# Kernel tuning notes

Measured on AMD Instinct MI355X. Metric: run time of the kernel, lower is better.

The kernel has to match this reference:

```python
import jax, jax.numpy as jnp
import numpy as np

V, D, T_BLK, H, L = 32000, 1024, 1024, 8 * 2, 8
HD = D // H
B, T = 4, 1024
EPS = 1e-5


def _ln(x, g, b):
    mu = jnp.mean(x, axis=-1, keepdims=True)
    var = jnp.mean(jnp.square(x - mu), axis=-1, keepdims=True)
    return (x - mu) * jax.lax.rsqrt(var + EPS) * g + b


def _forward(idx, tok_emb, pos_emb, Wq, Wk, Wv, Wo, bo, ln1_g, ln1_b, ln2_g, ln2_b,
             W1, b1, W2, b2, lnf_g, lnf_b, Whead, bhead):
    Bc, Tc = idx.shape
    x = tok_emb[idx] + pos_emb[:Tc]          # [B,T,D]
    mask = jnp.tril(jnp.ones((Tc, Tc), dtype=bool))
    scale = HD ** -0.5

    def block(x, p):
        wq, wk, wv, wo, bo_, g1, be1, g2, be2, w1, bf1, w2, bf2 = p
        xn = _ln(x, g1, be1)
        # per-head no-bias projections: wq/wk/wv are [H, D, HD]
        q = jnp.einsum('btd,hde->bhte', xn, wq)
        k = jnp.einsum('btd,hde->bhte', xn, wk)
        v = jnp.einsum('btd,hde->bhte', xn, wv)
        scores = jnp.einsum('bhte,bhse->bhts', q, k) * scale
        scores = jnp.where(mask, scores, -jnp.inf)
        w = jax.nn.softmax(scores, axis=-1)
        o = jnp.einsum('bhts,bhse->bhte', w, v)             # [B,H,T,HD]
        o = o.transpose(0, 2, 1, 3).reshape(Bc, Tc, D)       # concat heads
        x = x + jnp.einsum('btd,de->bte', o, wo) + bo_
        xn2 = _ln(x, g2, be2)
        h = jax.nn.gelu(jnp.einsum('btd,df->btf', xn2, w1) + bf1, approximate=False)
        x = x + jnp.einsum('btf,fd->btd', h, w2) + bf2
        return x, None

    x, _ = jax.lax.scan(block, x, (Wq, Wk, Wv, Wo, bo, ln1_g, ln1_b, ln2_g, ln2_b,
                                   W1, b1, W2, b2))
    x = _ln(x, lnf_g, lnf_b)
    logits = jnp.einsum('btd,dv->btv', x, Whead) + bhead
    return logits


def setup_inputs() -> dict:
    key = jax.random.key(0)
    ks = jax.random.split(key, 16)
    s = 0.02
    inp = {
        'idx': jax.random.randint(ks[0], (B, T), 0, V),
        'tok_emb': jax.random.normal(ks[1], (V, D), jnp.float32) * s,
        'pos_emb': jax.random.normal(ks[2], (T_BLK, D), jnp.float32) * s,
        'Wq': jax.random.normal(ks[3], (L, H, D, HD), jnp.float32) * s,
        'Wk': jax.random.normal(ks[4], (L, H, D, HD), jnp.float32) * s,
        'Wv': jax.random.normal(ks[5], (L, H, D, HD), jnp.float32) * s,
        'Wo': jax.random.normal(ks[6], (L, D, D), jnp.float32) * s,
        'bo': jnp.zeros((L, D), jnp.float32),
        'ln1_g': jnp.ones((L, D), jnp.float32),
        'ln1_b': jnp.zeros((L, D), jnp.float32),
        'ln2_g': jnp.ones((L, D), jnp.float32),
        'ln2_b': jnp.zeros((L, D), jnp.float32),
        'W1': jax.random.normal(ks[7], (L, D, 4 * D), jnp.float32) * s,
        'b1': jnp.zeros((L, 4 * D), jnp.float32),
        'W2': jax.random.normal(ks[8], (L, 4 * D, D), jnp.float32) * s,
        'b2': jnp.zeros((L, D), jnp.float32),
        'lnf_g': jnp.ones((D,), jnp.float32),
        'lnf_b': jnp.zeros((D,), jnp.float32),
        'Whead': jax.random.normal(ks[9], (D, V), jnp.float32) * s,
        'bhead': jnp.zeros((V,), jnp.float32),
    }
    return inp


def reference(idx, tok_emb, pos_emb, Wq, Wk, Wv, Wo, bo, ln1_g, ln1_b, ln2_g, ln2_b,
              W1, b1, W2, b2, lnf_g, lnf_b, Whead, bhead):
    return _forward(idx, tok_emb, pos_emb, Wq, Wk, Wv, Wo, bo, ln1_g, ln1_b,
                    ln2_g, ln2_b, W1, b1, W2, b2, lnf_g, lnf_b, Whead, bhead)
```

## Files before the change

### kernel.cpp

```cpp
#include <hip/hip_runtime.h>
#include <hip/hip_bf16.h>

typedef short bf16x8 __attribute__((ext_vector_type(8)));
typedef float f32x4 __attribute__((ext_vector_type(4)));

__device__ __forceinline__ unsigned short f2bf(float f) {
  union { float f; unsigned u; } un; un.f = f;
  unsigned r = un.u + 0x7fffu + ((un.u >> 16) & 1u);
  return (unsigned short)(r >> 16);
}

__device__ __forceinline__ void gl_lds16(const void* g, void* l) {
  __builtin_amdgcn_global_load_lds(
      (const __attribute__((address_space(1))) void*)g,
      (__attribute__((address_space(3))) void*)l, 16, 0, 0);
}

__global__ __launch_bounds__(256) void embed_k(const int* __restrict__ idx,
                                               const float* __restrict__ tok,
                                               const float* __restrict__ pos,
                                               float* __restrict__ x) {
  int m = blockIdx.x, t = threadIdx.x;
  int tk = idx[m];
  int tp = m & 1023;
  float4 a = ((const float4*)(tok + (long)tk * 1024))[t];
  float4 p = ((const float4*)(pos + (long)tp * 1024))[t];
  a.x += p.x; a.y += p.y; a.z += p.z; a.w += p.w;
  ((float4*)(x + (long)m * 1024))[t] = a;
}

__global__ __launch_bounds__(256) void ln_k(const float* __restrict__ x,
                                            const float* __restrict__ g,
                                            const float* __restrict__ b,
                                            unsigned short* __restrict__ out) {
  int row = blockIdx.x, t = threadIdx.x;
  float4 v = ((const float4*)(x + (long)row * 1024))[t];
  float s = v.x + v.y + v.z + v.w;
  float ss = v.x * v.x + v.y * v.y + v.z * v.z + v.w * v.w;
#pragma unroll
  for (int d = 32; d; d >>= 1) { s += __shfl_xor(s, d, 64); ss += __shfl_xor(ss, d, 64); }
  __shared__ float red[8];
  int wave = t >> 6, lane = t & 63;
  if (lane == 0) { red[wave] = s; red[wave + 4] = ss; }
  __syncthreads();
  s = red[0] + red[1] + red[2] + red[3];
  ss = red[4] + red[5] + red[6] + red[7];
  float mu = s * (1.f / 1024.f);
  float var = ss * (1.f / 1024.f) - mu * mu;
  float rstd = rsqrtf(var + 1e-5f);
  float4 gv = ((const float4*)g)[t];
  float4 bv = ((const float4*)b)[t];
  ushort4 o;
  o.x = f2bf((v.x - mu) * rstd * gv.x + bv.x);
  o.y = f2bf((v.y - mu) * rstd * gv.y + bv.y);
  o.z = f2bf((v.z - mu) * rstd * gv.z + bv.z);
  o.w = f2bf((v.w - mu) * rstd * gv.w + bv.w);
  ((ushort4*)(out + (long)row * 1024))[t] = o;
}

__global__ __launch_bounds__(256) void tr_k(const float* __restrict__ in,
                                            unsigned short* __restrict__ out,
                                            int R, int C, long inStride, long outStride) {
  __shared__ float tile[32][33];
  int batch = blockIdx.z;
  int c0 = blockIdx.x * 32, r0 = blockIdx.y * 32;
  const float* ip = in + (long)batch * inStride;
  unsigned short* op = out + (long)batch * outStride;
  int tx = threadIdx.x, ty = threadIdx.y;
#pragma unroll
  for (int i = 0; i < 4; ++i)
    tile[ty + i * 8][tx] = ip[(long)(r0 + ty + i * 8) * C + c0 + tx];
  __syncthreads();
#pragma unroll
  for (int i = 0; i < 4; ++i)
    op[(long)(c0 + ty + i * 8) * R + r0 + tx] = f2bf(tile[tx][ty + i * 8]);
}

__global__ __launch_bounds__(256) void tr_qkv_k(const float* __restrict__ wq,
                                                const float* __restrict__ wk,
                                                const float* __restrict__ wv,
                                                unsigned short* __restrict__ out) {
  __shared__ float tile[32][33];
  int z = blockIdx.z;
  int tsel = z >> 7, rem = z & 127;
  int l = rem >> 4, h = rem & 15;
  const float* ip = (tsel == 0 ? wq : tsel == 1 ? wk : wv) + (long)rem * 65536;
  unsigned short* op = out + (long)l * (3072 * 1024) + (long)tsel * (1024 * 1024) +
                       (long)h * 65536;
  int c0 = blockIdx.x * 32, r0 = blockIdx.y * 32;
  int tx = threadIdx.x, ty = threadIdx.y;
#pragma unroll
  for (int i = 0; i < 4; ++i)
    tile[ty + i * 8][tx] = ip[(long)(r0 + ty + i * 8) * 64 + c0 + tx];
  __syncthreads();
#pragma unroll
  for (int i = 0; i < 4; ++i)
    op[(long)(c0 + ty + i * 8) * 1024 + r0 + tx] = f2bf(tile[tx][ty + i * 8]);
}

template <int EPI>
__global__ __launch_bounds__(256) void gemm_bt(const unsigned short* __restrict__ A,
                                               const unsigned short* __restrict__ Bt,
                                               float* __restrict__ outf,
                                               unsigned short* __restrict__ outb,
                                               const float* __restrict__ bias,
                                               const float* __restrict__ res,
                                               int M, int N, int K) {
  __shared__ __align__(16) unsigned short sA[128 * 64];
  __shared__ __align__(16) unsigned short sB[128 * 64];
  const int t = threadIdx.x;
  const int wave = t >> 6, lane = t & 63;

  const int gx = gridDim.x;
  const int nwg = gx * gridDim.y;
  const int bid = blockIdx.y * gx + blockIdx.x;
  const int qd = nwg >> 3, rd = nwg & 7;
  const int xcd = bid & 7, off = bid >> 3;
  const int swz = (xcd < rd ? xcd * (qd + 1) : rd * (qd + 1) + (xcd - rd) * qd) + off;
  const int m0 = (swz / gx) << 7, n0 = (swz % gx) << 7;

  const int wm = (wave >> 1) * 64, wn = (wave & 1) * 64;
  const f32x4 z4 = {0.f, 0.f, 0.f, 0.f};
  f32x4 acc[4][4];
#pragma unroll
  for (int i = 0; i < 4; ++i)
#pragma unroll
    for (int j = 0; j < 4; ++j) acc[i][j] = z4;

  const int srow = t >> 3;
  const int scb = (((t & 7) ^ ((t >> 3) & 7)) << 4);
  const char* Ab = (const char*)A;
  const char* Bb = (const char*)Bt;
  char* sAb = (char*)sA;
  char* sBb = (char*)sB;
  const long ldb2 = (long)K * 2;
  const int pc0 = (((lane >> 4) ^ (lane & 7)) << 4);

  for (int k0 = 0; k0 < K; k0 += 64) {
    __syncthreads();
#pragma unroll
    for (int i = 0; i < 4; ++i) {
      int row = i * 32 + srow;
      gl_lds16(Ab + (long)(m0 + row) * ldb2 + (long)k0 * 2 + scb,
               sAb + i * 4096 + wave * 1024);
      gl_lds16(Bb + (long)(n0 + row) * ldb2 + (long)k0 * 2 + scb,
               sBb + i * 4096 + wave * 1024);
    }
    __syncthreads();
#pragma unroll
    for (int kk = 0; kk < 2; ++kk) {
      const int kb = pc0 ^ (kk << 6);
      bf16x8 af[4], bfr[4];
#pragma unroll
      for (int f = 0; f < 4; ++f) {
        int ra = wm + f * 16 + (lane & 15);
        af[f] = *(const bf16x8*)(sAb + ra * 128 + kb);
        int rb = wn + f * 16 + (lane & 15);
        bfr[f] = *(const bf16x8*)(sBb + rb * 128 + kb);
      }
#pragma unroll
      for (int fm = 0; fm < 4; ++fm)
#pragma unroll
        for (int fn = 0; fn < 4; ++fn)
          acc[fm][fn] = __builtin_amdgcn_mfma_f32_16x16x32_bf16(af[fm], bfr[fn], acc[fm][fn], 0, 0, 0);
    }
  }
  const int rl = (lane >> 4) << 2;
  const int cl = lane & 15;
#pragma unroll
  for (int fm = 0; fm < 4; ++fm) {
#pragma unroll
    for (int fn = 0; fn < 4; ++fn) {
#pragma unroll
      for (int r = 0; r < 4; ++r) {
        int m = m0 + wm + fm * 16 + rl + r;
        int n = n0 + wn + fn * 16 + cl;
        float v = acc[fm][fn][r];
        if (EPI == 1 || EPI == 2 || EPI == 3) v += bias[n];
        if (EPI == 1) v += res[(long)m * N + n];
        if (EPI == 2) v = 0.5f * v * (1.f + erff(v * 0.70710678118f));
        if (EPI == 0 || EPI == 2) outb[(long)m * N + n] = f2bf(v);
        else outf[(long)m * N + n] = v;
      }
    }
  }
}

__global__ __launch_bounds__(256) void attn_k(const unsigned short* __restrict__ qkv,
                                              unsigned short* __restrict__ o) {
  const int qt = blockIdx.x;
  const int pair = blockIdx.y;
  const int b = pair >> 4, h = pair & 15;
  const int t = threadIdx.x, wave = t >> 6, lane = t & 63;
  __shared__ __align__(16) unsigned short sQ[64 * 64];
  __shared__ __align__(16) unsigned short sK[64 * 64];
  __shared__ __align__(16) unsigned short sV[64 * 64];
  __shared__ __align__(16) unsigned short sP[4][16 * 64];

  const long baseq = (long)b * (1024 * 3072) + (long)h * 64;
  const unsigned short* qp = qkv + baseq;
  const unsigned short* kp = qkv + baseq + 1024;
  const unsigned short* vp = qkv + baseq + 2048;
  const long baseo = (long)b * (1024 * 1024) + (long)h * 64;

  {
    int c = t;
#pragma unroll
    for (int it = 0; it < 2; ++it, c += 256) {
      int row = c >> 3, e0 = (c & 7) << 3;
      bf16x8 val = *(const bf16x8*)(qp + (long)(qt * 64 + row) * 3072 + e0);
      *(bf16x8*)((char*)sQ + row * 128 + ((e0 * 2) ^ ((row & 7) << 4))) = val;
    }
  }

  float mst[4], lst[4];
  const f32x4 z4 = {0.f, 0.f, 0.f, 0.f};
  f32x4 oacc[4];
#pragma unroll
  for (int r = 0; r < 4; ++r) { mst[r] = -1e30f; lst[r] = 0.f; }
#pragma unroll
  for (int eb = 0; eb < 4; ++eb) oacc[eb] = z4;

  for (int kt = 0; kt <= qt; ++kt) {
    __syncthreads();
    {
      int c = t;
#pragma unroll
      for (int it = 0; it < 2; ++it, c += 256) {
        int row = c >> 3, e0 = (c & 7) << 3;
        bf16x8 kv = *(const bf16x8*)(kp + (long)(kt * 64 + row) * 3072 + e0);
        *(bf16x8*)((char*)sK + row * 128 + ((e0 * 2) ^ ((row & 7) << 4))) = kv;
        bf16x8 vv = *(const bf16x8*)(vp + (long)(kt * 64 + row) * 3072 + e0);
#pragma unroll
        for (int j = 0; j < 8; ++j) {
          int e = e0 + j;
          *(unsigned short*)((char*)sV + e * 128 + ((row * 2) ^ ((e & 7) << 4))) =
              (unsigned short)vv[j];
        }
      }
    }
    __syncthreads();

    f32x4 sf[4];
#pragma unroll
    for (int cb = 0; cb < 4; ++cb) {
      f32x4 s = z4;
#pragma unroll
      for (int kk = 0; kk < 2; ++kk) {
        int e0 = (kk * 32 + ((lane >> 4) << 3)) * 2;
        int qr = wave * 16 + (lane & 15);
        bf16x8 aq = *(const bf16x8*)((char*)sQ + qr * 128 + (e0 ^ ((qr & 7) << 4)));
        int kr = cb * 16 + (lane & 15);
        bf16x8 bk = *(const bf16x8*)((char*)sK + kr * 128 + (e0 ^ ((kr & 7) << 4)));
        s = __builtin_amdgcn_mfma_f32_16x16x32_bf16(aq, bk, s, 0, 0, 0);
      }
      sf[cb] = s;
    }

    const bool diag = (kt == qt);
#pragma unroll
    for (int r = 0; r < 4; ++r) {
      int qg = wave * 16 + ((lane >> 4) << 2) + r;
      float mx = -1e30f;
#pragma unroll
      for (int cb = 0; cb < 4; ++cb) {
        float sv = sf[cb][r] * 0.125f;
        if (diag) {
          int kg = cb * 16 + (lane & 15);
          if (kg > qg) sv = -1e30f;
        }
        sf[cb][r] = sv;
        mx = fmaxf(mx, sv);
      }
#pragma unroll
      for (int d = 1; d < 16; d <<= 1) mx = fmaxf(mx, __shfl_xor(mx, d, 64));
      float mnew = fmaxf(mst[r], mx);
      float corr = __expf(mst[r] - mnew);
      mst[r] = mnew;
      float rs = 0.f;
#pragma unroll
      for (int cb = 0; cb < 4; ++cb) {
        float p = __expf(sf[cb][r] - mnew);
        sf[cb][r] = p;
        rs += p;
      }
#pragma unroll
      for (int d = 1; d < 16; d <<= 1) rs += __shfl_xor(rs, d, 64);
      lst[r] = lst[r] * corr + rs;
#pragma unroll
      for (int eb = 0; eb < 4; ++eb) oacc[eb][r] *= corr;
    }

    unsigned short* pb = sP[wave];
#pragma unroll
    for (int r = 0; r < 4; ++r) {
      int lr = ((lane >> 4) << 2) + r;
#pragma unroll
      for (int cb = 0; cb < 4; ++cb) {
        int col = cb * 16 + (lane & 15);
        *(unsigned short*)((char*)pb + lr * 128 + ((col * 2) ^ ((lr & 7) << 4))) =
            f2bf(sf[cb][r]);
      }
    }

#pragma unroll
    for (int eb = 0; eb < 4; ++eb) {
#pragma unroll
      for (int kk = 0; kk < 2; ++kk) {
        int j0 = (kk * 32 + ((lane >> 4) << 3)) * 2;
        int pr = lane & 15;
        bf16x8 ap = *(const bf16x8*)((char*)pb + pr * 128 + (j0 ^ ((pr & 7) << 4)));
        int er = eb * 16 + (lane & 15);
        bf16x8 bv = *(const bf16x8*)((char*)sV + er * 128 + (j0 ^ ((er & 7) << 4)));
        oacc[eb] = __builtin_amdgcn_mfma_f32_16x16x32_bf16(ap, bv, oacc[eb], 0, 0, 0);
      }
    }
  }

#pragma unroll
  for (int r = 0; r < 4; ++r) {
    float inv = 1.f / lst[r];
    int qg = qt * 64 + wave * 16 + ((lane >> 4) << 2) + r;
#pragma unroll
    for (int eb = 0; eb < 4; ++eb) {
      int e = eb * 16 + (lane & 15);
      o[baseo + (long)qg * 1024 + e] = f2bf(oacc[eb][r] * inv);
    }
  }
}

extern "C" void kernel_launch(void* const* d_in, const int* in_sizes, int n_in,
                              void* d_out, int out_size, void* d_ws, size_t ws_size,
                              hipStream_t stream) {
  const int* idx = (const int*)d_in[0];
  const float* tok = (const float*)d_in[1];
  const float* pos = (const float*)d_in[2];
  const float* Wq = (const float*)d_in[3];
  const float* Wk = (const float*)d_in[4];
  const float* Wv = (const float*)d_in[5];
  const float* Wo = (const float*)d_in[6];
  const float* bo = (const float*)d_in[7];
  const float* ln1g = (const float*)d_in[8];
  const float* ln1b = (const float*)d_in[9];
  const float* ln2g = (const float*)d_in[10];
  const float* ln2b = (const float*)d_in[11];
  const float* W1 = (const float*)d_in[12];
  const float* b1 = (const float*)d_in[13];
  const float* W2 = (const float*)d_in[14];
  const float* b2 = (const float*)d_in[15];
  const float* lnfg = (const float*)d_in[16];
  const float* lnfb = (const float*)d_in[17];
  const float* Wh = (const float*)d_in[18];
  const float* bh = (const float*)d_in[19];

  char* ws = (char*)d_ws;
  const long Mi = 1024 * 1024;
  float* x = (float*)ws;
  unsigned short* xn = (unsigned short*)(ws + 16 * Mi);
  unsigned short* qkv = (unsigned short*)(ws + 24 * Mi);
  unsigned short* ob = (unsigned short*)(ws + 48 * Mi);
  unsigned short* hmid = (unsigned short*)(ws + 24 * Mi);
  unsigned short* wqkvT = (unsigned short*)(ws + 56 * Mi);
  unsigned short* wot = (unsigned short*)(ws + 104 * Mi);
  unsigned short* w1t = (unsigned short*)(ws + 106 * Mi);
  unsigned short* w2t = (unsigned short*)(ws + 114 * Mi);
  unsigned short* whT = (unsigned short*)(ws + 56 * Mi);

  dim3 blk256(256), blkT(32, 8);

  embed_k<<<4096, blk256, 0, stream>>>(idx, tok, pos, x);
  tr_qkv_k<<<dim3(2, 32, 384), blkT, 0, stream>>>(Wq, Wk, Wv, wqkvT);

  for (int l = 0; l < 8; ++l) {
    const float* wo_l = Wo + (long)l * 1048576;
    const float* w1_l = W1 + (long)l * 4194304;
    const float* w2_l = W2 + (long)l * 4194304;
    const float* bo_l = bo + (long)l * 1024;
    const float* b1_l = b1 + (long)l * 4096;
    const float* b2_l = b2 + (long)l * 1024;
    const unsigned short* wqkv_l = wqkvT + (long)l * (3072 * 1024);

    tr_k<<<dim3(32, 32, 1), blkT, 0, stream>>>(wo_l, wot, 1024, 1024, 0, 0);
    tr_k<<<dim3(128, 32, 1), blkT, 0, stream>>>(w1_l, w1t, 1024, 4096, 0, 0);
    tr_k<<<dim3(32, 128, 1), blkT, 0, stream>>>(w2_l, w2t, 4096, 1024, 0, 0);

    ln_k<<<4096, blk256, 0, stream>>>(x, ln1g + l * 1024, ln1b + l * 1024, xn);

    gemm_bt<0><<<dim3(24, 32), blk256, 0, stream>>>(xn, wqkv_l, nullptr, qkv, nullptr, nullptr, 4096, 3072, 1024);

    attn_k<<<dim3(16, 64), blk256, 0, stream>>>(qkv, ob);

    gemm_bt<1><<<dim3(8, 32), blk256, 0, stream>>>(ob, wot, x, nullptr, bo_l, x, 4096, 1024, 1024);

    ln_k<<<4096, blk256, 0, stream>>>(x, ln2g + l * 1024, ln2b + l * 1024, xn);

    gemm_bt<2><<<dim3(32, 32), blk256, 0, stream>>>(xn, w1t, nullptr, hmid, b1_l, nullptr, 4096, 4096, 1024);
    gemm_bt<1><<<dim3(8, 32), blk256, 0, stream>>>(hmid, w2t, x, nullptr, b2_l, x, 4096, 1024, 4096);
  }

  ln_k<<<4096, blk256, 0, stream>>>(x, lnfg, lnfb, xn);
  tr_k<<<dim3(1000, 32, 1), blkT, 0, stream>>>(Wh, whT, 1024, 32000, 0, 0);
  gemm_bt<3><<<dim3(250, 32), blk256, 0, stream>>>(xn, whT, (float*)d_out, nullptr, bh, nullptr, 4096, 32000, 1024);
}
```

Measured before the change: 2.904 ms.

## Add 256x256 tile, 8-wave GEMM with 4-stage LDS pipeline for QKV/FFN1/head

Adds a 512-thread GEMM kernel that computes 256x256 output tiles. It uses a four-deep global-to-LDS prefetch ring with split A/B staging, XCD-aware block swizzling and MFMA priority hints. The QKV, FFN up-projection and LM-head GEMMs move to it, and gemm_bt's epilogue is trimmed to the residual and bf16 cases it still serves. The aim is more data reuse per tile and better latency hiding, at the cost of high register and LDS use (one block per CU) and fewer blocks for small grids.

```diff
diff --git a/kernel.cpp b/kernel.cpp
--- a/kernel.cpp
+++ b/kernel.cpp
@@ -176,11 +176,131 @@
         int m = m0 + wm + fm * 16 + rl + r;
         int n = n0 + wn + fn * 16 + cl;
         float v = acc[fm][fn][r];
-        if (EPI == 1 || EPI == 2 || EPI == 3) v += bias[n];
-        if (EPI == 1) v += res[(long)m * N + n];
+        if (EPI == 1) v += bias[n] + res[(long)m * N + n];
+        if (EPI == 1) outf[(long)m * N + n] = v;
+        else outb[(long)m * N + n] = f2bf(v);
+      }
+    }
+  }
+}
+
+template <int EPI>
+__global__ __launch_bounds__(512, 1) void gemm256(const unsigned short* __restrict__ A,
+                                                  const unsigned short* __restrict__ Bt,
+                                                  float* __restrict__ outf,
+                                                  unsigned short* __restrict__ outb,
+                                                  const float* __restrict__ bias,
+                                                  int M, int N, int K) {
+  __shared__ __align__(16) char smem[131072];
+  const int t = threadIdx.x;
+  const int wave = t >> 6, lane = t & 63;
+
+  const int gx = gridDim.x;
+  const int nwg = gx * gridDim.y;
+  const int bid = blockIdx.y * gx + blockIdx.x;
+  const int qd = nwg >> 3, rd = nwg & 7;
+  const int xcd = bid & 7, off = bid >> 3;
+  const int swz = (xcd < rd ? xcd * (qd + 1) : rd * (qd + 1) + (xcd - rd) * qd) + off;
+  const int m0 = (swz / gx) << 8, n0 = (swz % gx) << 8;
+
+  const int wm = (wave >> 2) << 7;
+  const int wn = (wave & 3) << 6;
+  const int KT = K >> 5;
+
+  const f32x4 z4 = {0.f, 0.f, 0.f, 0.f};
+  f32x4 acc[8][4];
+#pragma unroll
+  for (int i = 0; i < 8; ++i)
+#pragma unroll
+    for (int j = 0; j < 4; ++j) acc[i][j] = z4;
+
+  const int srow = t >> 2;
+  const int sck = (((t & 3) ^ ((t >> 3) & 3)) << 4);
+  const long ldb = (long)K * 2;
+  const char* Asrc = (const char*)A + (long)(m0 + srow) * ldb + sck;
+  const char* Asrc2 = Asrc + 128 * ldb;
+  const char* Bsrc = (const char*)Bt + (long)(n0 + srow) * ldb + sck;
+  const char* Bsrc2 = Bsrc + 128 * ldb;
+
+#define STAGE_A(tt)                                                     \
+  { char* d = smem + ((tt) & 3) * 32768 + wave * 1024;                  \
+    long ko = (long)(tt) * 64;                                          \
+    gl_lds16(Asrc + ko, d); gl_lds16(Asrc2 + ko, d + 8192); }
+#define STAGE_B(tt)                                                     \
+  { char* d = smem + ((tt) & 3) * 32768 + 16384 + wave * 1024;          \
+    long ko = (long)(tt) * 64;                                          \
+    gl_lds16(Bsrc + ko, d); gl_lds16(Bsrc2 + ko, d + 8192); }
+
+  STAGE_A(0); STAGE_B(0);
+  STAGE_A(1); STAGE_B(1);
+  STAGE_A(2); STAGE_B(2);
+  asm volatile("s_waitcnt vmcnt(8)" ::: "memory");
+  __builtin_amdgcn_sched_barrier(0);
+  __builtin_amdgcn_s_barrier();
+
+  const int pck16 = (((lane >> 4) ^ ((lane >> 1) & 3)) << 4);
+  const int la15 = lane & 15;
+
+  for (int tt = 0; tt < KT; ++tt) {
+    const char* bA = smem + (tt & 3) * 32768;
+    const char* bB = bA + 16384;
+    bf16x8 af[4], bfr[4];
+
+#pragma unroll
+    for (int f = 0; f < 4; ++f)
+      af[f] = *(const bf16x8*)(bA + (wm + f * 16 + la15) * 64 + pck16);
+#pragma unroll
+    for (int g = 0; g < 4; ++g)
+      bfr[g] = *(const bf16x8*)(bB + (wn + g * 16 + la15) * 64 + pck16);
+    if (tt + 3 < KT) STAGE_A(tt + 3);
+    __builtin_amdgcn_s_barrier();
+    __builtin_amdgcn_s_setprio(1);
+#pragma unroll
+    for (int fm = 0; fm < 4; ++fm)
+#pragma unroll
+      for (int fn = 0; fn < 4; ++fn)
+        acc[fm][fn] = __builtin_amdgcn_mfma_f32_16x16x32_bf16(af[fm], bfr[fn], acc[fm][fn], 0, 0, 0);
+    __builtin_amdgcn_s_setprio(0);
+    __builtin_amdgcn_s_barrier();
+
+#pragma unroll
+    for (int f = 0; f < 4; ++f)
+      af[f] = *(const bf16x8*)(bA + (wm + (f + 4) * 16 + la15) * 64 + pck16);
+    if (tt + 3 < KT) STAGE_B(tt + 3);
+    __builtin_amdgcn_s_barrier();
+    __builtin_amdgcn_s_setprio(1);
+#pragma unroll
+    for (int fm = 0; fm < 4; ++fm)
+#pragma unroll
+      for (int fn = 0; fn < 4; ++fn)
+        acc[fm + 4][fn] = __builtin_amdgcn_mfma_f32_16x16x32_bf16(af[fm], bfr[fn], acc[fm + 4][fn], 0, 0, 0);
+    __builtin_amdgcn_s_setprio(0);
+
+    if (tt + 1 < KT) {
+      if (tt + 3 < KT)      asm volatile("s_waitcnt vmcnt(8)" ::: "memory");
+      else if (tt + 2 < KT) asm volatile("s_waitcnt vmcnt(4)" ::: "memory");
+      else                  asm volatile("s_waitcnt vmcnt(0)" ::: "memory");
+      __builtin_amdgcn_sched_barrier(0);
+    }
+    __builtin_amdgcn_s_barrier();
+  }
+#undef STAGE_A
+#undef STAGE_B
+
+  const int rl = (lane >> 4) << 2;
+#pragma unroll
+  for (int fm = 0; fm < 8; ++fm) {
+#pragma unroll
+    for (int fn = 0; fn < 4; ++fn) {
+#pragma unroll
+      for (int r = 0; r < 4; ++r) {
+        int m = m0 + wm + fm * 16 + rl + r;
+        int n = n0 + wn + fn * 16 + la15;
+        float v = acc[fm][fn][r];
+        if (EPI == 2 || EPI == 3) v += bias[n];
         if (EPI == 2) v = 0.5f * v * (1.f + erff(v * 0.70710678118f));
-        if (EPI == 0 || EPI == 2) outb[(long)m * N + n] = f2bf(v);
-        else outf[(long)m * N + n] = v;
+        if (EPI == 3) outf[(long)m * N + n] = v;
+        else outb[(long)m * N + n] = f2bf(v);
       }
     }
   }
@@ -366,7 +486,7 @@
   unsigned short* w2t = (unsigned short*)(ws + 114 * Mi);
   unsigned short* whT = (unsigned short*)(ws + 56 * Mi);
 
-  dim3 blk256(256), blkT(32, 8);
+  dim3 blk256(256), blk512(512), blkT(32, 8);
 
   embed_k<<<4096, blk256, 0, stream>>>(idx, tok, pos, x);
   tr_qkv_k<<<dim3(2, 32, 384), blkT, 0, stream>>>(Wq, Wk, Wv, wqkvT);
@@ -386,7 +506,7 @@
 
     ln_k<<<4096, blk256, 0, stream>>>(x, ln1g + l * 1024, ln1b + l * 1024, xn);
 
-    gemm_bt<0><<<dim3(24, 32), blk256, 0, stream>>>(xn, wqkv_l, nullptr, qkv, nullptr, nullptr, 4096, 3072, 1024);
+    gemm256<0><<<dim3(12, 16), blk512, 0, stream>>>(xn, wqkv_l, nullptr, qkv, nullptr, 4096, 3072, 1024);
 
     attn_k<<<dim3(16, 64), blk256, 0, stream>>>(qkv, ob);
 
@@ -394,11 +514,11 @@
 
     ln_k<<<4096, blk256, 0, stream>>>(x, ln2g + l * 1024, ln2b + l * 1024, xn);
 
-    gemm_bt<2><<<dim3(32, 32), blk256, 0, stream>>>(xn, w1t, nullptr, hmid, b1_l, nullptr, 4096, 4096, 1024);
+    gemm256<2><<<dim3(16, 16), blk512, 0, stream>>>(xn, w1t, nullptr, hmid, b1_l, 4096, 4096, 1024);
     gemm_bt<1><<<dim3(8, 32), blk256, 0, stream>>>(hmid, w2t, x, nullptr, b2_l, x, 4096, 1024, 4096);
   }
 
   ln_k<<<4096, blk256, 0, stream>>>(x, lnfg, lnfb, xn);
   tr_k<<<dim3(1000, 32, 1), blkT, 0, stream>>>(Wh, whT, 1024, 32000, 0, 0);
-  gemm_bt<3><<<dim3(250, 32), blk256, 0, stream>>>(xn, whT, (float*)d_out, nullptr, bh, nullptr, 4096, 32000, 1024);
-}
+  gemm256<3><<<dim3(125, 16), blk512, 0, stream>>>(xn, whT, (float*)d_out, nullptr, bh, 4096, 32000, 1024);
+}
```

Result: faster. 2.832 ms (-2.5%).
